# Kernel optimization log

Hardware: AMD Instinct MI355X
Metric: run time of the kernel (lower is better)

## Reference

```python
import jax, jax.numpy as jnp
import numpy as np

N_NODES = 10000
N_EDGES = 80000
F_NODE = 16
F_EDGE = 8
BN_EPS = 1e-5


def _nnconv(x, src, dst, edge_attr, w1, b1, w2, b2, w_root, bias, cin, cout):
    # edge MLP -> per-edge weight matrices [E, cin, cout]
    h = jax.nn.relu(edge_attr @ w1 + b1) @ w2 + b2
    w = h.reshape(-1, cin, cout)
    # gather source node features, per-edge matmul
    msg = jnp.einsum('ei,eio->eo', x[src], w)  # [E, cout]
    # scatter-mean into target nodes
    deg = jax.ops.segment_sum(jnp.ones(msg.shape[0], x.dtype), dst, num_segments=N_NODES)
    agg = jax.ops.segment_sum(msg, dst, num_segments=N_NODES) / jnp.clip(deg, 1.0)[:, None]
    return x @ w_root + agg + bias


def _batchnorm(x, gamma, beta):
    m = jnp.mean(x, axis=0)
    v = jnp.mean((x - m) ** 2, axis=0)  # biased var, as torch BN training mode
    return (x - m) * jax.lax.rsqrt(v + BN_EPS) * gamma + beta


def setup_inputs() -> dict:
    key = jax.random.key(0)
    ks = jax.random.split(key, 24)
    s = 0.05
    inp = {
        'x': jax.random.normal(ks[0], (N_NODES, F_NODE), jnp.float32),
        'edge_index': jax.random.randint(ks[1], (2, N_EDGES), 0, N_NODES, jnp.int32),
        'edge_attr': jax.random.normal(ks[2], (N_EDGES, F_EDGE), jnp.float32),
        # conv1 edge MLP: F_EDGE -> 25 -> 32*F_NODE
        'nn1_w1': jax.random.normal(ks[3], (F_EDGE, 25), jnp.float32) * s,
        'nn1_b1': jnp.zeros((25,), jnp.float32),
        'nn1_w2': jax.random.normal(ks[4], (25, 32 * F_NODE), jnp.float32) * s,
        'nn1_b2': jnp.zeros((32 * F_NODE,), jnp.float32),
        'conv1_root': jax.random.normal(ks[5], (F_NODE, 32), jnp.float32) * s,
        'conv1_bias': jnp.zeros((32,), jnp.float32),
        'bn1_gamma': jnp.ones((32,), jnp.float32),
        'bn1_beta': jnp.zeros((32,), jnp.float32),
        # conv2 edge MLP: F_EDGE -> 25 -> 32*64
        'nn2_w1': jax.random.normal(ks[6], (F_EDGE, 25), jnp.float32) * s,
        'nn2_b1': jnp.zeros((25,), jnp.float32),
        'nn2_w2': jax.random.normal(ks[7], (25, 32 * 64), jnp.float32) * s,
        'nn2_b2': jnp.zeros((32 * 64,), jnp.float32),
        'conv2_root': jax.random.normal(ks[8], (32, 64), jnp.float32) * s,
        'conv2_bias': jnp.zeros((64,), jnp.float32),
        'bn2_gamma': jnp.ones((64,), jnp.float32),
        'bn2_beta': jnp.zeros((64,), jnp.float32),
        'fc1_w': jax.random.normal(ks[9], (64, 128), jnp.float32) * s,
        'fc1_b': jnp.zeros((128,), jnp.float32),
        'fc2_w': jax.random.normal(ks[10], (128, 1), jnp.float32) * s,
        'fc2_b': jnp.zeros((1,), jnp.float32),
    }
    return inp


def reference(x, edge_index, edge_attr,
              nn1_w1, nn1_b1, nn1_w2, nn1_b2, conv1_root, conv1_bias, bn1_gamma, bn1_beta,
              nn2_w1, nn2_b1, nn2_w2, nn2_b2, conv2_root, conv2_bias, bn2_gamma, bn2_beta,
              fc1_w, fc1_b, fc2_w, fc2_b):
    src, dst = edge_index[0], edge_index[1]
    h = jax.nn.elu(_nnconv(x, src, dst, edge_attr, nn1_w1, nn1_b1, nn1_w2, nn1_b2,
                           conv1_root, conv1_bias, F_NODE, 32))
    h = jax.nn.elu(_batchnorm(h, bn1_gamma, bn1_beta))
    h = jax.nn.elu(_nnconv(h, src, dst, edge_attr, nn2_w1, nn2_b1, nn2_w2, nn2_b2,
                           conv2_root, conv2_bias, 32, 64))
    h = jax.nn.elu(_batchnorm(h, bn2_gamma, bn2_beta))
    h = jax.nn.elu(h @ fc1_w + fc1_b)
    h = jax.nn.elu(h @ fc2_w + fc2_b)  # [N, 1]
    # single graph: sum over all nodes -> shape [1]
    return jnp.sum(h).reshape(1)
```

## Files before the change

kernel.cpp:

```cpp
#include <hip/hip_runtime.h>
#include <hip/hip_bf16.h>
#include <hip/hip_fp16.h>

#define N_NODES 10000
#define N_EDGES 80000
#define FN 16
#define FE 8
#define HID 25
#define C1 32
#define C2 64
#define NU_BLOCKS 256
#define FC_BLOCKS 640
#define HROW 28
#define SLOTS 40
#define SC_BLOCKS ((N_EDGES + 255) / 256)
#define TN 25

typedef _Float16 h16;
typedef _Float16 h16x4 __attribute__((ext_vector_type(4)));

__device__ __forceinline__ float elu_f(float x) { return x > 0.f ? x : (expf(x) - 1.f); }

__device__ __forceinline__ float hdot(const h16* __restrict__ row, const float* Pk) {
    const h16x4* rv = (const h16x4*)row;
    float s = 0.f;
#pragma unroll
    for (int q = 0; q < 7; q++) {
        h16x4 hv = rv[q];
        s += (float)hv.x * Pk[4 * q] + (float)hv.y * Pk[4 * q + 1] +
             (float)hv.z * Pk[4 * q + 2] + (float)hv.w * Pk[4 * q + 3];
    }
    return s;
}

template <int CIN, int COUT>
__device__ __forceinline__ void pre_block(const float* __restrict__ xin,
                                          const float* __restrict__ w2,
                                          const float* __restrict__ b2,
                                          h16* __restrict__ P, int u, int tid) {
    constexpr int M = (HID + 1) * COUT;
    constexpr int MB = (M + 255) / 256;
    int mb = u % MB;
    int n0 = (u / MB) * TN;
    int m = mb * 256 + tid;
    if (m >= M) return;
    int k = m / COUT, o = m % COUT;
    float wreg[CIN];
    if (k < HID) {
#pragma unroll
        for (int i = 0; i < CIN; i++) wreg[i] = w2[(size_t)(k * CIN + i) * COUT + o];
    } else {
#pragma unroll
        for (int i = 0; i < CIN; i++) wreg[i] = b2[i * COUT + o];
    }
    for (int n = n0; n < n0 + TN; n++) {
        const float* xr = xin + (size_t)n * CIN;
        float s = 0.f;
#pragma unroll
        for (int i = 0; i < CIN; i++) s += xr[i] * wreg[i];
        P[(size_t)n * M + m] = (h16)s;
    }
}

__global__ void k_scatter_pre1(const float* __restrict__ ea, const int* __restrict__ ei,
                               const float* __restrict__ w1a, const float* __restrict__ b1a,
                               const float* __restrict__ w1b, const float* __restrict__ b1b,
                               const float* __restrict__ x, const float* __restrict__ w2a,
                               const float* __restrict__ b2a,
                               int* __restrict__ cnt_src, int* __restrict__ cnt_dst,
                               int* __restrict__ ebuf, h16* __restrict__ h1r,
                               h16* __restrict__ h2r, h16* __restrict__ P1) {
    int tid = threadIdx.x;
    int bid = blockIdx.x;
    if (bid >= SC_BLOCKS) {
        pre_block<FN, C1>(x, w2a, b2a, P1, bid - SC_BLOCKS, tid);
        return;
    }
    __shared__ float sw1a[FE * HID], sw1b[FE * HID], sb1a[HID], sb1b[HID];
    for (int i = tid; i < FE * HID; i += 256) { sw1a[i] = w1a[i]; sw1b[i] = w1b[i]; }
    if (tid < HID) { sb1a[tid] = b1a[tid]; sb1b[tid] = b1b[tid]; }
    __syncthreads();
    int e = bid * 256 + tid;
    if (e >= N_EDGES) return;
    float a[FE];
#pragma unroll
    for (int i = 0; i < FE; i++) a[i] = ea[e * FE + i];
    int src = ei[e], dst = ei[N_EDGES + e];
    int slot = atomicAdd(&cnt_src[src], 1);
    ebuf[src * SLOTS + slot] = (e << 14) | dst;
    atomicAdd(&cnt_dst[dst], 1);
    h16 b1buf[HROW], b2buf[HROW];
#pragma unroll
    for (int k = 0; k < HID; k++) {
        float s1 = sb1a[k], s2 = sb1b[k];
#pragma unroll
        for (int i = 0; i < FE; i++) { s1 += a[i] * sw1a[i * HID + k]; s2 += a[i] * sw1b[i * HID + k]; }
        b1buf[k] = (h16)fmaxf(s1, 0.f);
        b2buf[k] = (h16)fmaxf(s2, 0.f);
    }
    b1buf[25] = (h16)1.f; b1buf[26] = (h16)0.f; b1buf[27] = (h16)0.f;
    b2buf[25] = (h16)1.f; b2buf[26] = (h16)0.f; b2buf[27] = (h16)0.f;
    h16x4* h1p = (h16x4*)(h1r + (size_t)e * HROW);
    h16x4* h2p = (h16x4*)(h2r + (size_t)e * HROW);
#pragma unroll
    for (int q = 0; q < 7; q++) {
        h1p[q] = ((const h16x4*)b1buf)[q];
        h2p[q] = ((const h16x4*)b2buf)[q];
    }
}

template <int CIN, int COUT>
__global__ void k_precompute(const float* __restrict__ xin, const float* __restrict__ w2,
                             const float* __restrict__ b2, h16* __restrict__ P) {
    pre_block<CIN, COUT>(xin, w2, b2, P, blockIdx.x, threadIdx.x);
}

__global__ void k_msg_c1(const h16* __restrict__ P, const int* __restrict__ cnt_src,
                         const int* __restrict__ ebuf, const h16* __restrict__ h1r,
                         float* __restrict__ agg) {
    constexpr int M = (HID + 1) * C1;
    int lane = threadIdx.x & 63;
    int o = lane & 31;
    int n = __builtin_amdgcn_readfirstlane(blockIdx.x * 4 + (threadIdx.x >> 6));
    if (n >= N_NODES) return;
    const h16* Pr = P + (size_t)n * M;
    float Pk[HROW];
#pragma unroll
    for (int k = 0; k <= HID; k++) Pk[k] = (float)Pr[k * C1 + o];
    Pk[26] = 0.f; Pk[27] = 0.f;
    int beg = n * SLOTS, end = beg + cnt_src[n];
    int idx = beg;
    for (; idx + 3 < end; idx += 4) {
        int p0 = ebuf[idx], p1 = ebuf[idx + 1], p2 = ebuf[idx + 2], p3 = ebuf[idx + 3];
        float s0 = hdot(h1r + (size_t)(p0 >> 14) * HROW, Pk);
        float s1 = hdot(h1r + (size_t)(p1 >> 14) * HROW, Pk);
        float s2 = hdot(h1r + (size_t)(p2 >> 14) * HROW, Pk);
        float s3 = hdot(h1r + (size_t)(p3 >> 14) * HROW, Pk);
        float va = (lane < 32) ? s0 : s1;
        int da = (lane < 32) ? (p0 & 0x3FFF) : (p1 & 0x3FFF);
        atomicAdd(&agg[da * C1 + o], va);
        float vb = (lane < 32) ? s2 : s3;
        int db = (lane < 32) ? (p2 & 0x3FFF) : (p3 & 0x3FFF);
        atomicAdd(&agg[db * C1 + o], vb);
    }
    for (; idx + 1 < end; idx += 2) {
        int p0 = ebuf[idx], p1 = ebuf[idx + 1];
        float s0 = hdot(h1r + (size_t)(p0 >> 14) * HROW, Pk);
        float s1 = hdot(h1r + (size_t)(p1 >> 14) * HROW, Pk);
        float va = (lane < 32) ? s0 : s1;
        int da = (lane < 32) ? (p0 & 0x3FFF) : (p1 & 0x3FFF);
        atomicAdd(&agg[da * C1 + o], va);
    }
    if (idx < end) {
        int p0 = ebuf[idx];
        float s0 = hdot(h1r + (size_t)(p0 >> 14) * HROW, Pk);
        if (lane < 32) atomicAdd(&agg[(p0 & 0x3FFF) * C1 + o], s0);
    }
}

__global__ void k_msg_c2(const h16* __restrict__ P, const int* __restrict__ cnt_src,
                         const int* __restrict__ ebuf, const h16* __restrict__ h2r,
                         float* __restrict__ agg) {
    constexpr int M = (HID + 1) * C2;
    int lane = threadIdx.x & 63;
    int n = __builtin_amdgcn_readfirstlane(blockIdx.x * 4 + (threadIdx.x >> 6));
    if (n >= N_NODES) return;
    const h16* Pr = P + (size_t)n * M;
    float Pk[HROW];
#pragma unroll
    for (int k = 0; k <= HID; k++) Pk[k] = (float)Pr[k * C2 + lane];
    Pk[26] = 0.f; Pk[27] = 0.f;
    int beg = n * SLOTS, end = beg + cnt_src[n];
    int idx = beg;
    for (; idx + 3 < end; idx += 4) {
        int p0 = ebuf[idx], p1 = ebuf[idx + 1], p2 = ebuf[idx + 2], p3 = ebuf[idx + 3];
        float s0 = hdot(h2r + (size_t)(p0 >> 14) * HROW, Pk);
        float s1 = hdot(h2r + (size_t)(p1 >> 14) * HROW, Pk);
        float s2 = hdot(h2r + (size_t)(p2 >> 14) * HROW, Pk);
        float s3 = hdot(h2r + (size_t)(p3 >> 14) * HROW, Pk);
        atomicAdd(&agg[(p0 & 0x3FFF) * C2 + lane], s0);
        atomicAdd(&agg[(p1 & 0x3FFF) * C2 + lane], s1);
        atomicAdd(&agg[(p2 & 0x3FFF) * C2 + lane], s2);
        atomicAdd(&agg[(p3 & 0x3FFF) * C2 + lane], s3);
    }
    for (; idx < end; idx++) {
        int p0 = ebuf[idx];
        float s0 = hdot(h2r + (size_t)(p0 >> 14) * HROW, Pk);
        atomicAdd(&agg[(p0 & 0x3FFF) * C2 + lane], s0);
    }
}

template <int CIN, int COUT>
__global__ void k_node_update(const float* __restrict__ xin, const float* __restrict__ root,
                              const float* __restrict__ bias, const float* __restrict__ agg,
                              const int* __restrict__ degi, float* __restrict__ act,
                              float* __restrict__ s1g, float* __restrict__ s2g,
                              float* zero_out) {
    __shared__ float l1[256], l2[256];
    int tid = threadIdx.x;
    if (zero_out && blockIdx.x == 0 && tid == 0) *zero_out = 0.f;
    int o = tid % COUT;
    float b = bias[o];
    float rcol[CIN];
#pragma unroll
    for (int i = 0; i < CIN; i++) rcol[i] = root[i * COUT + o];
    float acc1 = 0.f, acc2 = 0.f;
    for (int t = blockIdx.x * 256 + tid; t < N_NODES * COUT; t += NU_BLOCKS * 256) {
        int n = t / COUT;
        const float* xr = xin + (size_t)n * CIN;
        float s = b;
#pragma unroll
        for (int i = 0; i < CIN; i++) s += xr[i] * rcol[i];
        s += agg[t] / fmaxf((float)degi[n], 1.0f);
        float a = elu_f(s);
        act[t] = a;
        acc1 += a; acc2 += a * a;
    }
    l1[tid] = acc1; l2[tid] = acc2;
    __syncthreads();
    for (int s = 128; s >= COUT; s >>= 1) {
        if (tid < s) { l1[tid] += l1[tid + s]; l2[tid] += l2[tid + s]; }
        __syncthreads();
    }
    if (tid < COUT) { atomicAdd(&s1g[tid], l1[tid]); atomicAdd(&s2g[tid], l2[tid]); }
}

template <int COUT>
__global__ void k_bn_elu(const float* __restrict__ act, const float* __restrict__ s1g,
                         const float* __restrict__ s2g, const float* __restrict__ gamma,
                         const float* __restrict__ beta, float* __restrict__ out) {
    int t = blockIdx.x * blockDim.x + threadIdx.x;
    if (t >= N_NODES * COUT) return;
    int o = t % COUT;
    float m = s1g[o] * (1.0f / N_NODES);
    float v = s2g[o] * (1.0f / N_NODES) - m * m;
    float x = (act[t] - m) * rsqrtf(v + 1e-5f) * gamma[o] + beta[o];
    out[t] = elu_f(x);
}

__global__ void k_fc_sum(const float* __restrict__ a2,
                         const float* __restrict__ s1g, const float* __restrict__ s2g,
                         const float* __restrict__ gamma, const float* __restrict__ beta,
                         const float* __restrict__ fc1w, const float* __restrict__ fc1b,
                         const float* __restrict__ fc2w, const float* __restrict__ fc2b,
                         float* __restrict__ out) {
    int tid = threadIdx.x;
    int lane = tid & 63;
    int wave = tid >> 6;
    float m = s1g[lane] * (1.0f / N_NODES);
    float var = s2g[lane] * (1.0f / N_NODES) - m * m;
    float scale = rsqrtf(var + 1e-5f) * gamma[lane];
    float shift = beta[lane] - m * scale;
    float b0 = fc1b[lane], b1 = fc1b[lane + 64];
    float w0 = fc2w[lane], w1 = fc2w[lane + 64];
    float fb = fc2b[0];
    float acc = 0.f;
    for (int n = blockIdx.x * 4 + wave; n < N_NODES; n += FC_BLOCKS * 4) {
        float hval = elu_f(a2[(size_t)n * C2 + lane] * scale + shift);
        float s0 = b0, s1 = b1;
#pragma unroll
        for (int i = 0; i < C2; i++) {
            float hv = __shfl(hval, i);
            s0 += hv * fc1w[i * 128 + lane];
            s1 += hv * fc1w[i * 128 + 64 + lane];
        }
        float v = elu_f(s0) * w0 + elu_f(s1) * w1;
#pragma unroll
        for (int off2 = 32; off2 > 0; off2 >>= 1) v += __shfl_down(v, off2);
        if (lane == 0) acc += elu_f(v + fb);
    }
    __shared__ float lds[4];
    if (lane == 0) lds[wave] = acc;
    __syncthreads();
    if (tid == 0) atomicAdd(out, lds[0] + lds[1] + lds[2] + lds[3]);
}

extern "C" void kernel_launch(void* const* d_in, const int* in_sizes, int n_in,
                              void* d_out, int out_size, void* d_ws, size_t ws_size,
                              hipStream_t stream) {
    const float* x       = (const float*)d_in[0];
    const int*   ei      = (const int*)d_in[1];
    const float* ea      = (const float*)d_in[2];
    const float* nn1_w1  = (const float*)d_in[3];
    const float* nn1_b1  = (const float*)d_in[4];
    const float* nn1_w2  = (const float*)d_in[5];
    const float* nn1_b2  = (const float*)d_in[6];
    const float* c1_root = (const float*)d_in[7];
    const float* c1_bias = (const float*)d_in[8];
    const float* bn1_g   = (const float*)d_in[9];
    const float* bn1_b   = (const float*)d_in[10];
    const float* nn2_w1  = (const float*)d_in[11];
    const float* nn2_b1  = (const float*)d_in[12];
    const float* nn2_w2  = (const float*)d_in[13];
    const float* nn2_b2  = (const float*)d_in[14];
    const float* c2_root = (const float*)d_in[15];
    const float* c2_bias = (const float*)d_in[16];
    const float* bn2_g   = (const float*)d_in[17];
    const float* bn2_b   = (const float*)d_in[18];
    const float* fc1_w   = (const float*)d_in[19];
    const float* fc1_b   = (const float*)d_in[20];
    const float* fc2_w   = (const float*)d_in[21];
    const float* fc2_b   = (const float*)d_in[22];
    float* out = (float*)d_out;

    char* ws = (char*)d_ws;
    size_t off = 0;
    auto alloc = [&](size_t nbytes) -> void* {
        void* q = (void*)(ws + off);
        off += nbytes;
        off = (off + 255) & ~(size_t)255;
        return q;
    };
    int*   cnt_src = (int*)alloc(N_NODES * 4);
    int*   cnt_dst = (int*)alloc(N_NODES * 4);
    float* agg1    = (float*)alloc((size_t)N_NODES * C1 * 4);
    float* agg2    = (float*)alloc((size_t)N_NODES * C2 * 4);
    float* bn1_s1  = (float*)alloc(C1 * 4);
    float* bn1_s2  = (float*)alloc(C1 * 4);
    float* bn2_s1  = (float*)alloc(C2 * 4);
    float* bn2_s2  = (float*)alloc(C2 * 4);
    size_t zero_bytes = off;
    int*   ebuf    = (int*)alloc((size_t)N_NODES * SLOTS * 4);
    h16*   h1r     = (h16*)alloc((size_t)N_EDGES * HROW * 2);
    h16*   h2r     = (h16*)alloc((size_t)N_EDGES * HROW * 2);
    h16*   P1      = (h16*)alloc((size_t)N_NODES * (HID + 1) * C1 * 2);
    h16*   P2      = (h16*)alloc((size_t)N_NODES * (HID + 1) * C2 * 2);
    float* a1      = (float*)alloc((size_t)N_NODES * C1 * 4);
    float* h1      = (float*)alloc((size_t)N_NODES * C1 * 4);
    float* a2      = (float*)alloc((size_t)N_NODES * C2 * 4);
    (void)ws_size; (void)in_sizes; (void)n_in; (void)out_size;

    hipMemsetAsync(d_ws, 0, zero_bytes, stream);

    constexpr int PRE1_BLOCKS = (((HID + 1) * C1 + 255) / 256) * (N_NODES / TN);
    constexpr int PRE2_BLOCKS = (((HID + 1) * C2 + 255) / 256) * (N_NODES / TN);

    k_scatter_pre1<<<SC_BLOCKS + PRE1_BLOCKS, 256, 0, stream>>>(
        ea, ei, nn1_w1, nn1_b1, nn2_w1, nn2_b1, x, nn1_w2, nn1_b2,
        cnt_src, cnt_dst, ebuf, h1r, h2r, P1);
    k_msg_c1<<<(N_NODES + 3) / 4, 256, 0, stream>>>(P1, cnt_src, ebuf, h1r, agg1);
    k_node_update<FN, C1><<<NU_BLOCKS, 256, 0, stream>>>(x, c1_root, c1_bias, agg1,
                                                         cnt_dst, a1, bn1_s1, bn1_s2, nullptr);
    k_bn_elu<C1><<<(N_NODES * C1) / 256, 256, 0, stream>>>(a1, bn1_s1, bn1_s2, bn1_g, bn1_b, h1);
    k_precompute<C1, C2><<<PRE2_BLOCKS, 256, 0, stream>>>(h1, nn2_w2, nn2_b2, P2);
    k_msg_c2<<<(N_NODES + 3) / 4, 256, 0, stream>>>(P2, cnt_src, ebuf, h2r, agg2);
    k_node_update<C1, C2><<<NU_BLOCKS, 256, 0, stream>>>(h1, c2_root, c2_bias, agg2,
                                                         cnt_dst, a2, bn2_s1, bn2_s2, out);
    k_fc_sum<<<FC_BLOCKS, 256, 0, stream>>>(a2, bn2_s1, bn2_s2, bn2_g, bn2_b,
                                            fc1_w, fc1_b, fc2_w, fc2_b, out);
}
```

Measured before the change: 244.3 us.

## Replace atomic scatter-add with per-edge message buffer and dst-CSR gather

```diff
diff --git a/kernel.cpp b/kernel.cpp
--- a/kernel.cpp
+++ b/kernel.cpp
@@ -9,7 +9,7 @@
 #define HID 25
 #define C1 32
 #define C2 64
-#define NU_BLOCKS 256
+#define NU_BLOCKS 768
 #define FC_BLOCKS 640
 #define HROW 28
 #define SLOTS 40
@@ -68,8 +68,9 @@
                                const float* __restrict__ x, const float* __restrict__ w2a,
                                const float* __restrict__ b2a,
                                int* __restrict__ cnt_src, int* __restrict__ cnt_dst,
-                               int* __restrict__ ebuf, h16* __restrict__ h1r,
-                               h16* __restrict__ h2r, h16* __restrict__ P1) {
+                               int* __restrict__ ebuf, int* __restrict__ ebuf_dst,
+                               h16* __restrict__ h1r, h16* __restrict__ h2r,
+                               h16* __restrict__ P1) {
     int tid = threadIdx.x;
     int bid = blockIdx.x;
     if (bid >= SC_BLOCKS) {
@@ -87,8 +88,9 @@
     for (int i = 0; i < FE; i++) a[i] = ea[e * FE + i];
     int src = ei[e], dst = ei[N_EDGES + e];
     int slot = atomicAdd(&cnt_src[src], 1);
-    ebuf[src * SLOTS + slot] = (e << 14) | dst;
-    atomicAdd(&cnt_dst[dst], 1);
+    if (slot < SLOTS) ebuf[src * SLOTS + slot] = (e << 14) | dst;
+    int slot2 = atomicAdd(&cnt_dst[dst], 1);
+    if (slot2 < SLOTS) ebuf_dst[dst * SLOTS + slot2] = e;
     h16 b1buf[HROW], b2buf[HROW];
 #pragma unroll
     for (int k = 0; k < HID; k++) {
@@ -117,7 +119,7 @@
 
 __global__ void k_msg_c1(const h16* __restrict__ P, const int* __restrict__ cnt_src,
                          const int* __restrict__ ebuf, const h16* __restrict__ h1r,
-                         float* __restrict__ agg) {
+                         float* __restrict__ msg) {
     constexpr int M = (HID + 1) * C1;
     int lane = threadIdx.x & 63;
     int o = lane & 31;
@@ -137,30 +139,30 @@
         float s2 = hdot(h1r + (size_t)(p2 >> 14) * HROW, Pk);
         float s3 = hdot(h1r + (size_t)(p3 >> 14) * HROW, Pk);
         float va = (lane < 32) ? s0 : s1;
-        int da = (lane < 32) ? (p0 & 0x3FFF) : (p1 & 0x3FFF);
-        atomicAdd(&agg[da * C1 + o], va);
+        int pa = (lane < 32) ? p0 : p1;
+        msg[(size_t)(pa >> 14) * C1 + o] = va;
         float vb = (lane < 32) ? s2 : s3;
-        int db = (lane < 32) ? (p2 & 0x3FFF) : (p3 & 0x3FFF);
-        atomicAdd(&agg[db * C1 + o], vb);
+        int pb = (lane < 32) ? p2 : p3;
+        msg[(size_t)(pb >> 14) * C1 + o] = vb;
     }
     for (; idx + 1 < end; idx += 2) {
         int p0 = ebuf[idx], p1 = ebuf[idx + 1];
         float s0 = hdot(h1r + (size_t)(p0 >> 14) * HROW, Pk);
         float s1 = hdot(h1r + (size_t)(p1 >> 14) * HROW, Pk);
         float va = (lane < 32) ? s0 : s1;
-        int da = (lane < 32) ? (p0 & 0x3FFF) : (p1 & 0x3FFF);
-        atomicAdd(&agg[da * C1 + o], va);
+        int pa = (lane < 32) ? p0 : p1;
+        msg[(size_t)(pa >> 14) * C1 + o] = va;
     }
     if (idx < end) {
         int p0 = ebuf[idx];
         float s0 = hdot(h1r + (size_t)(p0 >> 14) * HROW, Pk);
-        if (lane < 32) atomicAdd(&agg[(p0 & 0x3FFF) * C1 + o], s0);
+        if (lane < 32) msg[(size_t)(p0 >> 14) * C1 + o] = s0;
     }
 }
 
 __global__ void k_msg_c2(const h16* __restrict__ P, const int* __restrict__ cnt_src,
                          const int* __restrict__ ebuf, const h16* __restrict__ h2r,
-                         float* __restrict__ agg) {
+                         float* __restrict__ msg) {
     constexpr int M = (HID + 1) * C2;
     int lane = threadIdx.x & 63;
     int n = __builtin_amdgcn_readfirstlane(blockIdx.x * 4 + (threadIdx.x >> 6));
@@ -178,22 +180,23 @@
         float s1 = hdot(h2r + (size_t)(p1 >> 14) * HROW, Pk);
         float s2 = hdot(h2r + (size_t)(p2 >> 14) * HROW, Pk);
         float s3 = hdot(h2r + (size_t)(p3 >> 14) * HROW, Pk);
-        atomicAdd(&agg[(p0 & 0x3FFF) * C2 + lane], s0);
-        atomicAdd(&agg[(p1 & 0x3FFF) * C2 + lane], s1);
-        atomicAdd(&agg[(p2 & 0x3FFF) * C2 + lane], s2);
-        atomicAdd(&agg[(p3 & 0x3FFF) * C2 + lane], s3);
+        msg[(size_t)(p0 >> 14) * C2 + lane] = s0;
+        msg[(size_t)(p1 >> 14) * C2 + lane] = s1;
+        msg[(size_t)(p2 >> 14) * C2 + lane] = s2;
+        msg[(size_t)(p3 >> 14) * C2 + lane] = s3;
     }
     for (; idx < end; idx++) {
         int p0 = ebuf[idx];
         float s0 = hdot(h2r + (size_t)(p0 >> 14) * HROW, Pk);
-        atomicAdd(&agg[(p0 & 0x3FFF) * C2 + lane], s0);
+        msg[(size_t)(p0 >> 14) * C2 + lane] = s0;
     }
 }
 
 template <int CIN, int COUT>
 __global__ void k_node_update(const float* __restrict__ xin, const float* __restrict__ root,
-                              const float* __restrict__ bias, const float* __restrict__ agg,
-                              const int* __restrict__ degi, float* __restrict__ act,
+                              const float* __restrict__ bias, const float* __restrict__ msg,
+                              const int* __restrict__ ebuf_dst, const int* __restrict__ degi,
+                              float* __restrict__ act,
                               float* __restrict__ s1g, float* __restrict__ s2g,
                               float* zero_out) {
     __shared__ float l1[256], l2[256];
@@ -211,7 +214,17 @@
         float s = b;
 #pragma unroll
         for (int i = 0; i < CIN; i++) s += xr[i] * rcol[i];
-        s += agg[t] / fmaxf((float)degi[n], 1.0f);
+        int deg = degi[n];
+        int base = n * SLOTS;
+        float acc = 0.f;
+        for (int j = 0; j < deg; j += 4) {
+            int4 ee = *(const int4*)(ebuf_dst + base + j);
+            acc += msg[(size_t)ee.x * COUT + o];
+            if (j + 1 < deg) acc += msg[(size_t)ee.y * COUT + o];
+            if (j + 2 < deg) acc += msg[(size_t)ee.z * COUT + o];
+            if (j + 3 < deg) acc += msg[(size_t)ee.w * COUT + o];
+        }
+        s += acc / fmaxf((float)deg, 1.0f);
         float a = elu_f(s);
         act[t] = a;
         acc1 += a; acc2 += a * a;
@@ -313,21 +326,22 @@
     };
     int*   cnt_src = (int*)alloc(N_NODES * 4);
     int*   cnt_dst = (int*)alloc(N_NODES * 4);
-    float* agg1    = (float*)alloc((size_t)N_NODES * C1 * 4);
-    float* agg2    = (float*)alloc((size_t)N_NODES * C2 * 4);
     float* bn1_s1  = (float*)alloc(C1 * 4);
     float* bn1_s2  = (float*)alloc(C1 * 4);
     float* bn2_s1  = (float*)alloc(C2 * 4);
     float* bn2_s2  = (float*)alloc(C2 * 4);
     size_t zero_bytes = off;
-    int*   ebuf    = (int*)alloc((size_t)N_NODES * SLOTS * 4);
-    h16*   h1r     = (h16*)alloc((size_t)N_EDGES * HROW * 2);
-    h16*   h2r     = (h16*)alloc((size_t)N_EDGES * HROW * 2);
-    h16*   P1      = (h16*)alloc((size_t)N_NODES * (HID + 1) * C1 * 2);
-    h16*   P2      = (h16*)alloc((size_t)N_NODES * (HID + 1) * C2 * 2);
-    float* a1      = (float*)alloc((size_t)N_NODES * C1 * 4);
-    float* h1      = (float*)alloc((size_t)N_NODES * C1 * 4);
-    float* a2      = (float*)alloc((size_t)N_NODES * C2 * 4);
+    int*   ebuf     = (int*)alloc((size_t)N_NODES * SLOTS * 4);
+    int*   ebuf_dst = (int*)alloc((size_t)N_NODES * SLOTS * 4);
+    h16*   h1r      = (h16*)alloc((size_t)N_EDGES * HROW * 2);
+    h16*   h2r      = (h16*)alloc((size_t)N_EDGES * HROW * 2);
+    h16*   P1       = (h16*)alloc((size_t)N_NODES * (HID + 1) * C1 * 2);
+    h16*   P2       = (h16*)alloc((size_t)N_NODES * (HID + 1) * C2 * 2);
+    float* msg1     = (float*)alloc((size_t)N_EDGES * C1 * 4);
+    float* msg2     = (float*)alloc((size_t)N_EDGES * C2 * 4);
+    float* a1       = (float*)alloc((size_t)N_NODES * C1 * 4);
+    float* h1       = (float*)alloc((size_t)N_NODES * C1 * 4);
+    float* a2       = (float*)alloc((size_t)N_NODES * C2 * 4);
     (void)ws_size; (void)in_sizes; (void)n_in; (void)out_size;
 
     hipMemsetAsync(d_ws, 0, zero_bytes, stream);
@@ -337,15 +351,15 @@
 
     k_scatter_pre1<<<SC_BLOCKS + PRE1_BLOCKS, 256, 0, stream>>>(
         ea, ei, nn1_w1, nn1_b1, nn2_w1, nn2_b1, x, nn1_w2, nn1_b2,
-        cnt_src, cnt_dst, ebuf, h1r, h2r, P1);
-    k_msg_c1<<<(N_NODES + 3) / 4, 256, 0, stream>>>(P1, cnt_src, ebuf, h1r, agg1);
-    k_node_update<FN, C1><<<NU_BLOCKS, 256, 0, stream>>>(x, c1_root, c1_bias, agg1,
-                                                         cnt_dst, a1, bn1_s1, bn1_s2, nullptr);
+        cnt_src, cnt_dst, ebuf, ebuf_dst, h1r, h2r, P1);
+    k_msg_c1<<<(N_NODES + 3) / 4, 256, 0, stream>>>(P1, cnt_src, ebuf, h1r, msg1);
+    k_node_update<FN, C1><<<NU_BLOCKS, 256, 0, stream>>>(x, c1_root, c1_bias, msg1,
+                                                         ebuf_dst, cnt_dst, a1, bn1_s1, bn1_s2, nullptr);
     k_bn_elu<C1><<<(N_NODES * C1) / 256, 256, 0, stream>>>(a1, bn1_s1, bn1_s2, bn1_g, bn1_b, h1);
     k_precompute<C1, C2><<<PRE2_BLOCKS, 256, 0, stream>>>(h1, nn2_w2, nn2_b2, P2);
-    k_msg_c2<<<(N_NODES + 3) / 4, 256, 0, stream>>>(P2, cnt_src, ebuf, h2r, agg2);
-    k_node_update<C1, C2><<<NU_BLOCKS, 256, 0, stream>>>(h1, c2_root, c2_bias, agg2,
-                                                         cnt_dst, a2, bn2_s1, bn2_s2, out);
+    k_msg_c2<<<(N_NODES + 3) / 4, 256, 0, stream>>>(P2, cnt_src, ebuf, h2r, msg2);
+    k_node_update<C1, C2><<<NU_BLOCKS, 256, 0, stream>>>(h1, c2_root, c2_bias, msg2,
+                                                         ebuf_dst, cnt_dst, a2, bn2_s1, bn2_s2, out);
     k_fc_sum<<<FC_BLOCKS, 256, 0, stream>>>(a2, bn2_s1, bn2_s2, bn2_g, bn2_b,
                                             fc1_w, fc1_b, fc2_w, fc2_b, out);
 }
```

After: 266.1 us. +8.9%, slower.

## Fuse all GNN stages into one persistent cooperative kernel with grid syncs

Applied to the files above, without the earlier changes.

```diff
diff --git a/kernel.cpp b/kernel.cpp
--- a/kernel.cpp
+++ b/kernel.cpp
@@ -1,6 +1,8 @@
 #include <hip/hip_runtime.h>
-#include <hip/hip_bf16.h>
 #include <hip/hip_fp16.h>
+#include <hip/hip_cooperative_groups.h>
+
+namespace cg = cooperative_groups;
 
 #define N_NODES 10000
 #define N_EDGES 80000
@@ -9,12 +11,13 @@
 #define HID 25
 #define C1 32
 #define C2 64
+#define HROW 28
+#define SLOTS 40
+#define TN 25
+#define NB_MAX 512
 #define NU_BLOCKS 256
 #define FC_BLOCKS 640
-#define HROW 28
-#define SLOTS 40
 #define SC_BLOCKS ((N_EDGES + 255) / 256)
-#define TN 25
 
 typedef _Float16 h16;
 typedef _Float16 h16x4 __attribute__((ext_vector_type(4)));
@@ -34,96 +37,43 @@
 }
 
 template <int CIN, int COUT>
-__device__ __forceinline__ void pre_block(const float* __restrict__ xin,
-                                          const float* __restrict__ w2,
-                                          const float* __restrict__ b2,
-                                          h16* __restrict__ P, int u, int tid) {
+__device__ __forceinline__ void pre_unit(const float* __restrict__ xin,
+                                         const float* __restrict__ w2,
+                                         const float* __restrict__ b2,
+                                         h16* __restrict__ Pq, int u, int tid) {
     constexpr int M = (HID + 1) * COUT;
     constexpr int MB = (M + 255) / 256;
     int mb = u % MB;
     int n0 = (u / MB) * TN;
     int m = mb * 256 + tid;
-    if (m >= M) return;
-    int k = m / COUT, o = m % COUT;
-    float wreg[CIN];
-    if (k < HID) {
-#pragma unroll
-        for (int i = 0; i < CIN; i++) wreg[i] = w2[(size_t)(k * CIN + i) * COUT + o];
-    } else {
-#pragma unroll
-        for (int i = 0; i < CIN; i++) wreg[i] = b2[i * COUT + o];
-    }
-    for (int n = n0; n < n0 + TN; n++) {
-        const float* xr = xin + (size_t)n * CIN;
-        float s = 0.f;
-#pragma unroll
-        for (int i = 0; i < CIN; i++) s += xr[i] * wreg[i];
-        P[(size_t)n * M + m] = (h16)s;
-    }
-}
-
-__global__ void k_scatter_pre1(const float* __restrict__ ea, const int* __restrict__ ei,
-                               const float* __restrict__ w1a, const float* __restrict__ b1a,
-                               const float* __restrict__ w1b, const float* __restrict__ b1b,
-                               const float* __restrict__ x, const float* __restrict__ w2a,
-                               const float* __restrict__ b2a,
-                               int* __restrict__ cnt_src, int* __restrict__ cnt_dst,
-                               int* __restrict__ ebuf, h16* __restrict__ h1r,
-                               h16* __restrict__ h2r, h16* __restrict__ P1) {
-    int tid = threadIdx.x;
-    int bid = blockIdx.x;
-    if (bid >= SC_BLOCKS) {
-        pre_block<FN, C1>(x, w2a, b2a, P1, bid - SC_BLOCKS, tid);
-        return;
-    }
-    __shared__ float sw1a[FE * HID], sw1b[FE * HID], sb1a[HID], sb1b[HID];
-    for (int i = tid; i < FE * HID; i += 256) { sw1a[i] = w1a[i]; sw1b[i] = w1b[i]; }
-    if (tid < HID) { sb1a[tid] = b1a[tid]; sb1b[tid] = b1b[tid]; }
-    __syncthreads();
-    int e = bid * 256 + tid;
-    if (e >= N_EDGES) return;
-    float a[FE];
-#pragma unroll
-    for (int i = 0; i < FE; i++) a[i] = ea[e * FE + i];
-    int src = ei[e], dst = ei[N_EDGES + e];
-    int slot = atomicAdd(&cnt_src[src], 1);
-    ebuf[src * SLOTS + slot] = (e << 14) | dst;
-    atomicAdd(&cnt_dst[dst], 1);
-    h16 b1buf[HROW], b2buf[HROW];
-#pragma unroll
-    for (int k = 0; k < HID; k++) {
-        float s1 = sb1a[k], s2 = sb1b[k];
-#pragma unroll
-        for (int i = 0; i < FE; i++) { s1 += a[i] * sw1a[i * HID + k]; s2 += a[i] * sw1b[i * HID + k]; }
-        b1buf[k] = (h16)fmaxf(s1, 0.f);
-        b2buf[k] = (h16)fmaxf(s2, 0.f);
-    }
-    b1buf[25] = (h16)1.f; b1buf[26] = (h16)0.f; b1buf[27] = (h16)0.f;
-    b2buf[25] = (h16)1.f; b2buf[26] = (h16)0.f; b2buf[27] = (h16)0.f;
-    h16x4* h1p = (h16x4*)(h1r + (size_t)e * HROW);
-    h16x4* h2p = (h16x4*)(h2r + (size_t)e * HROW);
-#pragma unroll
-    for (int q = 0; q < 7; q++) {
-        h1p[q] = ((const h16x4*)b1buf)[q];
-        h2p[q] = ((const h16x4*)b2buf)[q];
-    }
-}
-
-template <int CIN, int COUT>
-__global__ void k_precompute(const float* __restrict__ xin, const float* __restrict__ w2,
-                             const float* __restrict__ b2, h16* __restrict__ P) {
-    pre_block<CIN, COUT>(xin, w2, b2, P, blockIdx.x, threadIdx.x);
-}
-
-__global__ void k_msg_c1(const h16* __restrict__ P, const int* __restrict__ cnt_src,
-                         const int* __restrict__ ebuf, const h16* __restrict__ h1r,
-                         float* __restrict__ agg) {
+    if (m < M) {
+        int k = m / COUT, o = m % COUT;
+        float wreg[CIN];
+        if (k < HID) {
+#pragma unroll
+            for (int i = 0; i < CIN; i++) wreg[i] = w2[(size_t)(k * CIN + i) * COUT + o];
+        } else {
+#pragma unroll
+            for (int i = 0; i < CIN; i++) wreg[i] = b2[i * COUT + o];
+        }
+        for (int n = n0; n < n0 + TN; n++) {
+            const float* xr = xin + (size_t)n * CIN;
+            float s = 0.f;
+#pragma unroll
+            for (int i = 0; i < CIN; i++) s += xr[i] * wreg[i];
+            Pq[(size_t)n * M + m] = (h16)s;
+        }
+    }
+}
+
+__device__ __forceinline__ void msg1_node(int n, const h16* __restrict__ Pp,
+                                          const int* __restrict__ cnt_src,
+                                          const int* __restrict__ ebuf,
+                                          const h16* __restrict__ h1r,
+                                          float* __restrict__ agg, int lane) {
     constexpr int M = (HID + 1) * C1;
-    int lane = threadIdx.x & 63;
     int o = lane & 31;
-    int n = __builtin_amdgcn_readfirstlane(blockIdx.x * 4 + (threadIdx.x >> 6));
-    if (n >= N_NODES) return;
-    const h16* Pr = P + (size_t)n * M;
+    const h16* Pr = Pp + (size_t)n * M;
     float Pk[HROW];
 #pragma unroll
     for (int k = 0; k <= HID; k++) Pk[k] = (float)Pr[k * C1 + o];
@@ -158,14 +108,13 @@
     }
 }
 
-__global__ void k_msg_c2(const h16* __restrict__ P, const int* __restrict__ cnt_src,
-                         const int* __restrict__ ebuf, const h16* __restrict__ h2r,
-                         float* __restrict__ agg) {
+__device__ __forceinline__ void msg2_node(int n, const h16* __restrict__ Pp,
+                                          const int* __restrict__ cnt_src,
+                                          const int* __restrict__ ebuf,
+                                          const h16* __restrict__ h2r,
+                                          float* __restrict__ agg, int lane) {
     constexpr int M = (HID + 1) * C2;
-    int lane = threadIdx.x & 63;
-    int n = __builtin_amdgcn_readfirstlane(blockIdx.x * 4 + (threadIdx.x >> 6));
-    if (n >= N_NODES) return;
-    const h16* Pr = P + (size_t)n * M;
+    const h16* Pr = Pp + (size_t)n * M;
     float Pk[HROW];
 #pragma unroll
     for (int k = 0; k <= HID; k++) Pk[k] = (float)Pr[k * C2 + lane];
@@ -188,6 +137,257 @@
         float s0 = hdot(h2r + (size_t)(p0 >> 14) * HROW, Pk);
         atomicAdd(&agg[(p0 & 0x3FFF) * C2 + lane], s0);
     }
+}
+
+
+struct Args {
+    const float *x, *ea;
+    const int* ei;
+    const float *w1a, *b1a, *w2a, *b2a, *c1_root, *c1_bias, *bn1_g, *bn1_b;
+    const float *w1b, *b1b, *w2b, *b2b, *c2_root, *c2_bias, *bn2_g, *bn2_b;
+    const float *fc1w, *fc1b, *fc2w, *fc2b;
+    int *cnt_src, *cnt_dst, *ebuf;
+    h16 *h1r, *h2r, *P1, *P2;
+    float *agg1, *agg2, *a1, *h1v, *a2;
+    float *bn1_s1, *bn1_s2, *bn2_s1, *bn2_s2;
+    float* out;
+    int nb;
+};
+
+__device__ __forceinline__ void gsync(cg::grid_group& g) {
+    __threadfence();
+    g.sync();
+}
+
+template <int CIN, int COUT>
+__device__ __forceinline__ void node_update_phase(const float* __restrict__ xin,
+                                                  const float* __restrict__ root,
+                                                  const float* __restrict__ bias,
+                                                  const float* __restrict__ agg,
+                                                  const int* __restrict__ degi,
+                                                  float* __restrict__ act,
+                                                  float* __restrict__ s1g, float* __restrict__ s2g,
+                                                  float* smem, int tid, int gtid, int nth) {
+    float* l1 = smem;
+    float* l2 = smem + 256;
+    int o = tid % COUT;
+    float b = bias[o];
+    float rcol[CIN];
+#pragma unroll
+    for (int i = 0; i < CIN; i++) rcol[i] = root[i * COUT + o];
+    float acc1 = 0.f, acc2 = 0.f;
+    for (int t = gtid; t < N_NODES * COUT; t += nth) {
+        int n = t / COUT;
+        const float* xr = xin + (size_t)n * CIN;
+        float s = b;
+#pragma unroll
+        for (int i = 0; i < CIN; i++) s += xr[i] * rcol[i];
+        s += agg[t] / fmaxf((float)degi[n], 1.0f);
+        float a = elu_f(s);
+        act[t] = a;
+        acc1 += a; acc2 += a * a;
+    }
+    l1[tid] = acc1; l2[tid] = acc2;
+    __syncthreads();
+    for (int s = 128; s >= COUT; s >>= 1) {
+        if (tid < s) { l1[tid] += l1[tid + s]; l2[tid] += l2[tid + s]; }
+        __syncthreads();
+    }
+    if (tid < COUT) { atomicAdd(&s1g[tid], l1[tid]); atomicAdd(&s2g[tid], l2[tid]); }
+    __syncthreads();
+}
+
+__global__ __launch_bounds__(256, 2) void fused(Args p) {
+    cg::grid_group grid = cg::this_grid();
+    __shared__ float smem[512];
+    int tid = threadIdx.x;
+    int bid = blockIdx.x;
+    int gtid = bid * 256 + tid;
+    int lane = tid & 63;
+    int nb = p.nb;
+    int nth = nb << 8;
+    int nwaves = nth >> 6;
+    int gwave = gtid >> 6;
+
+    constexpr int PRE1_UNITS = (((HID + 1) * C1 + 255) / 256) * (N_NODES / TN);
+    constexpr int PRE2_UNITS = (((HID + 1) * C2 + 255) / 256) * (N_NODES / TN);
+
+    {
+        float* sw1a = smem;
+        float* sw1b = smem + 200;
+        float* sb1a = smem + 400;
+        float* sb1b = smem + 425;
+        for (int i = tid; i < FE * HID; i += 256) { sw1a[i] = p.w1a[i]; sw1b[i] = p.w1b[i]; }
+        if (tid < HID) { sb1a[tid] = p.b1a[tid]; sb1b[tid] = p.b1b[tid]; }
+        __syncthreads();
+        if (gtid == 0) *p.out = 0.f;
+        for (int e = gtid; e < N_EDGES; e += nth) {
+            float a[FE];
+#pragma unroll
+            for (int i = 0; i < FE; i++) a[i] = p.ea[e * FE + i];
+            int src = p.ei[e], dst = p.ei[N_EDGES + e];
+            int slot = atomicAdd(&p.cnt_src[src], 1);
+            if (slot < SLOTS) p.ebuf[src * SLOTS + slot] = (e << 14) | dst;
+            atomicAdd(&p.cnt_dst[dst], 1);
+            h16 b1buf[HROW], b2buf[HROW];
+#pragma unroll
+            for (int k = 0; k < HID; k++) {
+                float s1 = sb1a[k], s2 = sb1b[k];
+#pragma unroll
+                for (int i = 0; i < FE; i++) {
+                    s1 += a[i] * sw1a[i * HID + k];
+                    s2 += a[i] * sw1b[i * HID + k];
+                }
+                b1buf[k] = (h16)fmaxf(s1, 0.f);
+                b2buf[k] = (h16)fmaxf(s2, 0.f);
+            }
+            b1buf[25] = (h16)1.f; b1buf[26] = (h16)0.f; b1buf[27] = (h16)0.f;
+            b2buf[25] = (h16)1.f; b2buf[26] = (h16)0.f; b2buf[27] = (h16)0.f;
+            h16x4* h1p = (h16x4*)(p.h1r + (size_t)e * HROW);
+            h16x4* h2p = (h16x4*)(p.h2r + (size_t)e * HROW);
+#pragma unroll
+            for (int q = 0; q < 7; q++) {
+                h1p[q] = ((const h16x4*)b1buf)[q];
+                h2p[q] = ((const h16x4*)b2buf)[q];
+            }
+        }
+        for (int u = bid; u < PRE1_UNITS; u += nb) pre_unit<FN, C1>(p.x, p.w2a, p.b2a, p.P1, u, tid);
+        __syncthreads();
+    }
+    gsync(grid);
+
+    for (int w = gwave; w < N_NODES; w += nwaves) {
+        int n = __builtin_amdgcn_readfirstlane(w);
+        msg1_node(n, p.P1, p.cnt_src, p.ebuf, p.h1r, p.agg1, lane);
+    }
+    gsync(grid);
+
+    node_update_phase<FN, C1>(p.x, p.c1_root, p.c1_bias, p.agg1, p.cnt_dst,
+                              p.a1, p.bn1_s1, p.bn1_s2, smem, tid, gtid, nth);
+    gsync(grid);
+
+    for (int t = gtid; t < N_NODES * C1; t += nth) {
+        int o = t % C1;
+        float m = p.bn1_s1[o] * (1.0f / N_NODES);
+        float v = p.bn1_s2[o] * (1.0f / N_NODES) - m * m;
+        float xv = (p.a1[t] - m) * rsqrtf(v + 1e-5f) * p.bn1_g[o] + p.bn1_b[o];
+        p.h1v[t] = elu_f(xv);
+    }
+    gsync(grid);
+
+    for (int u = bid; u < PRE2_UNITS; u += nb) pre_unit<C1, C2>(p.h1v, p.w2b, p.b2b, p.P2, u, tid);
+    gsync(grid);
+
+    for (int w = gwave; w < N_NODES; w += nwaves) {
+        int n = __builtin_amdgcn_readfirstlane(w);
+        msg2_node(n, p.P2, p.cnt_src, p.ebuf, p.h2r, p.agg2, lane);
+    }
+    gsync(grid);
+
+    node_update_phase<C1, C2>(p.h1v, p.c2_root, p.c2_bias, p.agg2, p.cnt_dst,
+                              p.a2, p.bn2_s1, p.bn2_s2, smem, tid, gtid, nth);
+    gsync(grid);
+
+    {
+        int wv = tid >> 6;
+        float m = p.bn2_s1[lane] * (1.0f / N_NODES);
+        float var = p.bn2_s2[lane] * (1.0f / N_NODES) - m * m;
+        float scale = rsqrtf(var + 1e-5f) * p.bn2_g[lane];
+        float shift = p.bn2_b[lane] - m * scale;
+        float b0 = p.fc1b[lane], b1 = p.fc1b[lane + 64];
+        float w0 = p.fc2w[lane], w1 = p.fc2w[lane + 64];
+        float fb = p.fc2b[0];
+        float acc = 0.f;
+        for (int n = gwave; n < N_NODES; n += nwaves) {
+            float hval = elu_f(p.a2[(size_t)n * C2 + lane] * scale + shift);
+            float s0 = b0, s1 = b1;
+#pragma unroll
+            for (int i = 0; i < C2; i++) {
+                float hv = __shfl(hval, i);
+                s0 += hv * p.fc1w[i * 128 + lane];
+                s1 += hv * p.fc1w[i * 128 + 64 + lane];
+            }
+            float v = elu_f(s0) * w0 + elu_f(s1) * w1;
+#pragma unroll
+            for (int off2 = 32; off2 > 0; off2 >>= 1) v += __shfl_down(v, off2);
+            if (lane == 0) acc += elu_f(v + fb);
+        }
+        if (lane == 0) smem[wv] = acc;
+        __syncthreads();
+        if (tid == 0) atomicAdd(p.out, smem[0] + smem[1] + smem[2] + smem[3]);
+    }
+}
+
+
+__global__ void k_scatter_pre1(const float* __restrict__ ea, const int* __restrict__ ei,
+                               const float* __restrict__ w1a, const float* __restrict__ b1a,
+                               const float* __restrict__ w1b, const float* __restrict__ b1b,
+                               const float* __restrict__ x, const float* __restrict__ w2a,
+                               const float* __restrict__ b2a,
+                               int* __restrict__ cnt_src, int* __restrict__ cnt_dst,
+                               int* __restrict__ ebuf, h16* __restrict__ h1r,
+                               h16* __restrict__ h2r, h16* __restrict__ P1) {
+    int tid = threadIdx.x;
+    int bid = blockIdx.x;
+    if (bid >= SC_BLOCKS) {
+        pre_unit<FN, C1>(x, w2a, b2a, P1, bid - SC_BLOCKS, tid);
+        return;
+    }
+    __shared__ float sw1a[FE * HID], sw1b[FE * HID], sb1a[HID], sb1b[HID];
+    for (int i = tid; i < FE * HID; i += 256) { sw1a[i] = w1a[i]; sw1b[i] = w1b[i]; }
+    if (tid < HID) { sb1a[tid] = b1a[tid]; sb1b[tid] = b1b[tid]; }
+    __syncthreads();
+    int e = bid * 256 + tid;
+    if (e >= N_EDGES) return;
+    float a[FE];
+#pragma unroll
+    for (int i = 0; i < FE; i++) a[i] = ea[e * FE + i];
+    int src = ei[e], dst = ei[N_EDGES + e];
+    int slot = atomicAdd(&cnt_src[src], 1);
+    if (slot < SLOTS) ebuf[src * SLOTS + slot] = (e << 14) | dst;
+    atomicAdd(&cnt_dst[dst], 1);
+    h16 b1buf[HROW], b2buf[HROW];
+#pragma unroll
+    for (int k = 0; k < HID; k++) {
+        float s1 = sb1a[k], s2 = sb1b[k];
+#pragma unroll
+        for (int i = 0; i < FE; i++) { s1 += a[i] * sw1a[i * HID + k]; s2 += a[i] * sw1b[i * HID + k]; }
+        b1buf[k] = (h16)fmaxf(s1, 0.f);
+        b2buf[k] = (h16)fmaxf(s2, 0.f);
+    }
+    b1buf[25] = (h16)1.f; b1buf[26] = (h16)0.f; b1buf[27] = (h16)0.f;
+    b2buf[25] = (h16)1.f; b2buf[26] = (h16)0.f; b2buf[27] = (h16)0.f;
+    h16x4* h1p = (h16x4*)(h1r + (size_t)e * HROW);
+    h16x4* h2p = (h16x4*)(h2r + (size_t)e * HROW);
+#pragma unroll
+    for (int q = 0; q < 7; q++) {
+        h1p[q] = ((const h16x4*)b1buf)[q];
+        h2p[q] = ((const h16x4*)b2buf)[q];
+    }
+}
+
+template <int CIN, int COUT>
+__global__ void k_precompute(const float* __restrict__ xin, const float* __restrict__ w2,
+                             const float* __restrict__ b2, h16* __restrict__ P) {
+    pre_unit<CIN, COUT>(xin, w2, b2, P, blockIdx.x, threadIdx.x);
+}
+
+__global__ void k_msg_c1(const h16* __restrict__ P, const int* __restrict__ cnt_src,
+                         const int* __restrict__ ebuf, const h16* __restrict__ h1r,
+                         float* __restrict__ agg) {
+    int lane = threadIdx.x & 63;
+    int n = __builtin_amdgcn_readfirstlane(blockIdx.x * 4 + (threadIdx.x >> 6));
+    if (n >= N_NODES) return;
+    msg1_node(n, P, cnt_src, ebuf, h1r, agg, lane);
+}
+
+__global__ void k_msg_c2(const h16* __restrict__ P, const int* __restrict__ cnt_src,
+                         const int* __restrict__ ebuf, const h16* __restrict__ h2r,
+                         float* __restrict__ agg) {
+    int lane = threadIdx.x & 63;
+    int n = __builtin_amdgcn_readfirstlane(blockIdx.x * 4 + (threadIdx.x >> 6));
+    if (n >= N_NODES) return;
+    msg2_node(n, P, cnt_src, ebuf, h2r, agg, lane);
 }
 
 template <int CIN, int COUT>
@@ -275,33 +475,35 @@
     if (tid == 0) atomicAdd(out, lds[0] + lds[1] + lds[2] + lds[3]);
 }
 
+
 extern "C" void kernel_launch(void* const* d_in, const int* in_sizes, int n_in,
                               void* d_out, int out_size, void* d_ws, size_t ws_size,
                               hipStream_t stream) {
-    const float* x       = (const float*)d_in[0];
-    const int*   ei      = (const int*)d_in[1];
-    const float* ea      = (const float*)d_in[2];
-    const float* nn1_w1  = (const float*)d_in[3];
-    const float* nn1_b1  = (const float*)d_in[4];
-    const float* nn1_w2  = (const float*)d_in[5];
-    const float* nn1_b2  = (const float*)d_in[6];
-    const float* c1_root = (const float*)d_in[7];
-    const float* c1_bias = (const float*)d_in[8];
-    const float* bn1_g   = (const float*)d_in[9];
-    const float* bn1_b   = (const float*)d_in[10];
-    const float* nn2_w1  = (const float*)d_in[11];
-    const float* nn2_b1  = (const float*)d_in[12];
-    const float* nn2_w2  = (const float*)d_in[13];
-    const float* nn2_b2  = (const float*)d_in[14];
-    const float* c2_root = (const float*)d_in[15];
-    const float* c2_bias = (const float*)d_in[16];
-    const float* bn2_g   = (const float*)d_in[17];
-    const float* bn2_b   = (const float*)d_in[18];
-    const float* fc1_w   = (const float*)d_in[19];
-    const float* fc1_b   = (const float*)d_in[20];
-    const float* fc2_w   = (const float*)d_in[21];
-    const float* fc2_b   = (const float*)d_in[22];
-    float* out = (float*)d_out;
+    Args a;
+    a.x       = (const float*)d_in[0];
+    a.ei      = (const int*)d_in[1];
+    a.ea      = (const float*)d_in[2];
+    a.w1a     = (const float*)d_in[3];
+    a.b1a     = (const float*)d_in[4];
+    a.w2a     = (const float*)d_in[5];
+    a.b2a     = (const float*)d_in[6];
+    a.c1_root = (const float*)d_in[7];
+    a.c1_bias = (const float*)d_in[8];
+    a.bn1_g   = (const float*)d_in[9];
+    a.bn1_b   = (const float*)d_in[10];
+    a.w1b     = (const float*)d_in[11];
+    a.b1b     = (const float*)d_in[12];
+    a.w2b     = (const float*)d_in[13];
+    a.b2b     = (const float*)d_in[14];
+    a.c2_root = (const float*)d_in[15];
+    a.c2_bias = (const float*)d_in[16];
+    a.bn2_g   = (const float*)d_in[17];
+    a.bn2_b   = (const float*)d_in[18];
+    a.fc1w    = (const float*)d_in[19];
+    a.fc1b    = (const float*)d_in[20];
+    a.fc2w    = (const float*)d_in[21];
+    a.fc2b    = (const float*)d_in[22];
+    a.out     = (float*)d_out;
 
     char* ws = (char*)d_ws;
     size_t off = 0;
@@ -311,41 +513,74 @@
         off = (off + 255) & ~(size_t)255;
         return q;
     };
-    int*   cnt_src = (int*)alloc(N_NODES * 4);
-    int*   cnt_dst = (int*)alloc(N_NODES * 4);
-    float* agg1    = (float*)alloc((size_t)N_NODES * C1 * 4);
-    float* agg2    = (float*)alloc((size_t)N_NODES * C2 * 4);
-    float* bn1_s1  = (float*)alloc(C1 * 4);
-    float* bn1_s2  = (float*)alloc(C1 * 4);
-    float* bn2_s1  = (float*)alloc(C2 * 4);
-    float* bn2_s2  = (float*)alloc(C2 * 4);
+    a.cnt_src = (int*)alloc(N_NODES * 4);
+    a.cnt_dst = (int*)alloc(N_NODES * 4);
+    a.agg1    = (float*)alloc((size_t)N_NODES * C1 * 4);
+    a.agg2    = (float*)alloc((size_t)N_NODES * C2 * 4);
+    a.bn1_s1  = (float*)alloc(C1 * 4);
+    a.bn1_s2  = (float*)alloc(C1 * 4);
+    a.bn2_s1  = (float*)alloc(C2 * 4);
+    a.bn2_s2  = (float*)alloc(C2 * 4);
     size_t zero_bytes = off;
-    int*   ebuf    = (int*)alloc((size_t)N_NODES * SLOTS * 4);
-    h16*   h1r     = (h16*)alloc((size_t)N_EDGES * HROW * 2);
-    h16*   h2r     = (h16*)alloc((size_t)N_EDGES * HROW * 2);
-    h16*   P1      = (h16*)alloc((size_t)N_NODES * (HID + 1) * C1 * 2);
-    h16*   P2      = (h16*)alloc((size_t)N_NODES * (HID + 1) * C2 * 2);
-    float* a1      = (float*)alloc((size_t)N_NODES * C1 * 4);
-    float* h1      = (float*)alloc((size_t)N_NODES * C1 * 4);
-    float* a2      = (float*)alloc((size_t)N_NODES * C2 * 4);
+    a.ebuf = (int*)alloc((size_t)N_NODES * SLOTS * 4);
+    a.h1r  = (h16*)alloc((size_t)N_EDGES * HROW * 2);
+    a.h2r  = (h16*)alloc((size_t)N_EDGES * HROW * 2);
+    a.P1   = (h16*)alloc((size_t)N_NODES * (HID + 1) * C1 * 2);
+    a.P2   = (h16*)alloc((size_t)N_NODES * (HID + 1) * C2 * 2);
+    a.a1   = (float*)alloc((size_t)N_NODES * C1 * 4);
+    a.h1v  = (float*)alloc((size_t)N_NODES * C1 * 4);
+    a.a2   = (float*)alloc((size_t)N_NODES * C2 * 4);
     (void)ws_size; (void)in_sizes; (void)n_in; (void)out_size;
 
     hipMemsetAsync(d_ws, 0, zero_bytes, stream);
 
-    constexpr int PRE1_BLOCKS = (((HID + 1) * C1 + 255) / 256) * (N_NODES / TN);
-    constexpr int PRE2_BLOCKS = (((HID + 1) * C2 + 255) / 256) * (N_NODES / TN);
-
-    k_scatter_pre1<<<SC_BLOCKS + PRE1_BLOCKS, 256, 0, stream>>>(
-        ea, ei, nn1_w1, nn1_b1, nn2_w1, nn2_b1, x, nn1_w2, nn1_b2,
-        cnt_src, cnt_dst, ebuf, h1r, h2r, P1);
-    k_msg_c1<<<(N_NODES + 3) / 4, 256, 0, stream>>>(P1, cnt_src, ebuf, h1r, agg1);
-    k_node_update<FN, C1><<<NU_BLOCKS, 256, 0, stream>>>(x, c1_root, c1_bias, agg1,
-                                                         cnt_dst, a1, bn1_s1, bn1_s2, nullptr);
-    k_bn_elu<C1><<<(N_NODES * C1) / 256, 256, 0, stream>>>(a1, bn1_s1, bn1_s2, bn1_g, bn1_b, h1);
-    k_precompute<C1, C2><<<PRE2_BLOCKS, 256, 0, stream>>>(h1, nn2_w2, nn2_b2, P2);
-    k_msg_c2<<<(N_NODES + 3) / 4, 256, 0, stream>>>(P2, cnt_src, ebuf, h2r, agg2);
-    k_node_update<C1, C2><<<NU_BLOCKS, 256, 0, stream>>>(h1, c2_root, c2_bias, agg2,
-                                                         cnt_dst, a2, bn2_s1, bn2_s2, out);
-    k_fc_sum<<<FC_BLOCKS, 256, 0, stream>>>(a2, bn2_s1, bn2_s2, bn2_g, bn2_b,
-                                            fc1_w, fc1_b, fc2_w, fc2_b, out);
-}
+    static int s_nb = -2;
+    if (s_nb == -2) {
+        int dev = 0;
+        (void)hipGetDevice(&dev);
+        int cus = 0;
+        (void)hipDeviceGetAttribute(&cus, hipDeviceAttributeMultiprocessorCount, dev);
+        int maxb = 0;
+        hipError_t qe = hipOccupancyMaxActiveBlocksPerMultiprocessor(&maxb, (const void*)fused, 256, 0);
+        if (qe != hipSuccess || cus <= 0 || maxb <= 0) {
+            s_nb = 0;
+        } else {
+            long nb = (long)maxb * (long)cus;
+            s_nb = (int)(nb > NB_MAX ? NB_MAX : nb);
+        }
+        (void)hipGetLastError();
+    }
+
+    bool launched = false;
+    if (s_nb > 0) {
+        a.nb = s_nb;
+        void* kargs[] = { (void*)&a };
+        hipError_t err = hipLaunchCooperativeKernel((const void*)fused, dim3(s_nb), dim3(256),
+                                                    kargs, 0, stream);
+        if (err == hipSuccess) {
+            launched = true;
+        } else {
+            s_nb = 0;
+            (void)hipGetLastError();
+        }
+    }
+
+    if (!launched) {
+        constexpr int PRE1_BLOCKS = (((HID + 1) * C1 + 255) / 256) * (N_NODES / TN);
+        constexpr int PRE2_BLOCKS = (((HID + 1) * C2 + 255) / 256) * (N_NODES / TN);
+        k_scatter_pre1<<<SC_BLOCKS + PRE1_BLOCKS, 256, 0, stream>>>(
+            a.ea, a.ei, a.w1a, a.b1a, a.w1b, a.b1b, a.x, a.w2a, a.b2a,
+            a.cnt_src, a.cnt_dst, a.ebuf, a.h1r, a.h2r, a.P1);
+        k_msg_c1<<<(N_NODES + 3) / 4, 256, 0, stream>>>(a.P1, a.cnt_src, a.ebuf, a.h1r, a.agg1);
+        k_node_update<FN, C1><<<NU_BLOCKS, 256, 0, stream>>>(a.x, a.c1_root, a.c1_bias, a.agg1,
+                                                             a.cnt_dst, a.a1, a.bn1_s1, a.bn1_s2, nullptr);
+        k_bn_elu<C1><<<(N_NODES * C1) / 256, 256, 0, stream>>>(a.a1, a.bn1_s1, a.bn1_s2,
+                                                               a.bn1_g, a.bn1_b, a.h1v);
+        k_precompute<C1, C2><<<PRE2_BLOCKS, 256, 0, stream>>>(a.h1v, a.w2b, a.b2b, a.P2);
+        k_msg_c2<<<(N_NODES + 3) / 4, 256, 0, stream>>>(a.P2, a.cnt_src, a.ebuf, a.h2r, a.agg2);
+        k_node_update<C1, C2><<<NU_BLOCKS, 256, 0, stream>>>(a.h1v, a.c2_root, a.c2_bias, a.agg2,
+                                                             a.cnt_dst, a.a2, a.bn2_s1, a.bn2_s2, a.out);
+        k_fc_sum<<<FC_BLOCKS, 256, 0, stream>>>(a.a2, a.bn2_s1, a.bn2_s2, a.bn2_g, a.bn2_b,
+                                                a.fc1w, a.fc1b, a.fc2w, a.fc2b, a.out);
+    }
+}
```

Result: slower. 746.7 us (+205.7%).
